# Optimization experiments

Measured on AMD Instinct MI355X. Metric: run time of the kernel, lower is better.

Reference implementation:

```python
import jax, jax.numpy as jnp
import numpy as np

N, E = 50000, 800000
C, NT, ET, H, D = 128, 8, 16, 64, 4
TOTAL_IN = 2 * C + 2 * NT + ET  # 288
EPS = 1e-5


def setup_inputs() -> dict:
    key = jax.random.key(0)
    ks = jax.random.split(key, 10)
    x = jax.random.normal(ks[0], (N, C), dtype=jnp.float32)
    edge_index = jax.random.randint(ks[1], (2, E), 0, N, dtype=jnp.int64)
    edge_types = jax.random.randint(ks[2], (E,), 0, ET, dtype=jnp.int64)
    node_types = jax.random.randint(ks[3], (N,), 0, NT, dtype=jnp.int64)
    ln_w = jnp.ones((TOTAL_IN,), dtype=jnp.float32)
    ln_b = jnp.zeros((TOTAL_IN,), dtype=jnp.float32)
    W1 = jax.random.normal(ks[4], (TOTAL_IN, H), dtype=jnp.float32) * 0.05
    b1 = jnp.zeros((H,), dtype=jnp.float32)
    W2 = jax.random.normal(ks[5], (H, D * D), dtype=jnp.float32) * 0.05
    b2 = jnp.zeros((D * D,), dtype=jnp.float32)
    return {"x": x, "edge_index": edge_index, "edge_types": edge_types,
            "node_types": node_types, "ln_w": ln_w, "ln_b": ln_b,
            "W1": W1, "b1": b1, "W2": W2, "b2": b2}


def reference(x, edge_index, edge_types, node_types, ln_w, ln_b, W1, b1, W2, b2):
    row, col = edge_index[0], edge_index[1]
    # edge gathers of node features and one-hot type encodings
    nt_oh = jax.nn.one_hot(node_types, NT, dtype=x.dtype)   # [N, NT]
    et_oh = jax.nn.one_hot(edge_types, ET, dtype=x.dtype)   # [E, ET]
    h = jnp.concatenate([x[row], x[col], nt_oh[row], nt_oh[col], et_oh], axis=-1)  # [E, 288]
    # LayerNorm
    mu = jnp.mean(h, axis=-1, keepdims=True)
    var = jnp.mean(jnp.square(h - mu), axis=-1, keepdims=True)
    h = (h - mu) * jax.lax.rsqrt(var + EPS) * ln_w + ln_b
    # small MLP
    h = jax.nn.relu(h @ W1 + b1) @ W2 + b2          # [E, D*D]
    h = h.reshape(-1, D, D)
    att = jax.nn.softmax(h, axis=-1)                 # row-stochastic per edge
    return jnp.eye(D, dtype=h.dtype)[None] - att     # [E, D, D]
```

## Files before the change

### kernel.cpp

```cpp
#include <hip/hip_runtime.h>
#include <hip/hip_bf16.h>

#define NN 50000
#define NE 800000
#define C 128
#define HH 64
#define TIN 288
#define LN_EPS 1e-5f

typedef __attribute__((ext_vector_type(8))) short bf16x8;
typedef __attribute__((ext_vector_type(4))) float f32x4;
typedef __attribute__((ext_vector_type(2))) float f32x2;
typedef __attribute__((ext_vector_type(4))) int i32x4;

#define ETT_OFF 512
#define B1F_OFF 2560
#define B2F_OFF 35328
#define OHU_OFF 37376
#define OHV_OFF 38400
#define SQ_OFF 39424
#define U_OFF 439424
#define V_OFF 3639424

__device__ __forceinline__ short f2bf(float f) {
    __hip_bfloat16 h = __float2bfloat16(f);
    return __builtin_bit_cast(short, h);
}
__device__ __forceinline__ float bf2f(short s) {
    unsigned int u = ((unsigned int)(unsigned short)s) << 16;
    return __builtin_bit_cast(float, u);
}

__global__ void prep_weights(const float* __restrict__ ln_w,
                             const float* __restrict__ ln_b,
                             const float* __restrict__ W1,
                             const float* __restrict__ b1,
                             const float* __restrict__ W2,
                             float* __restrict__ ws) {
    int gid = blockIdx.x * 256 + threadIdx.x;
    if (blockIdx.x == 0 && threadIdx.x < 64) {
        int l = threadIdx.x;
        float s = 0.f, c = 0.f;
        for (int k = 0; k < TIN; ++k) {
            float w = W1[k * HH + l];
            s += ln_w[k] * w;
            c += ln_b[k] * w;
        }
        ws[l] = s;
        ws[64 + l] = c + b1[l];
    }
    short* B1 = (short*)((char*)ws + B1F_OFF);
    for (int idx = gid; idx < 16384; idx += 8192) {
        int j = idx & 7, l = (idx >> 3) & 63, cc = (idx >> 9) & 3, kt = idx >> 11;
        int g = l >> 4, m = l & 15;
        int k = 32 * kt + 8 * g + j, n = 16 * cc + m;
        B1[idx] = f2bf(ln_w[k] * W1[k * HH + n]);
    }
    short* B2 = (short*)((char*)ws + B2F_OFF);
    for (int idx = gid; idx < 1024; idx += 8192) {
        int j = idx & 7, l = (idx >> 3) & 63, kt = idx >> 9;
        int g = l >> 4, m = l & 15;
        int k = 32 * kt + 8 * g + j;
        B2[idx] = f2bf(W2[k * 16 + m]);
    }
    short* ohu = (short*)((char*)ws + OHU_OFF);
    short* ohv = (short*)((char*)ws + OHV_OFF);
    for (int idx = gid; idx < 512; idx += 8192) {
        int t = idx >> 6, j = idx & 63;
        ohu[idx] = f2bf(ln_w[256 + t] * W1[(256 + t) * HH + j]);
        ohv[idx] = f2bf(ln_w[264 + t] * W1[(264 + t) * HH + j]);
    }
    short* ett = (short*)((char*)ws + ETT_OFF);
    for (int idx = gid; idx < 1024; idx += 8192) {
        int et = idx >> 6, j = idx & 63;
        int unit = (j >> 3) ^ (et & 7);
        ett[et * 64 + unit * 8 + (j & 7)] = f2bf(ln_w[272 + et] * W1[(272 + et) * HH + j]);
    }
}

__global__ __launch_bounds__(512) void node_uv(const float* __restrict__ x,
                                               const int* __restrict__ ntype,
                                               float* __restrict__ ws) {
    __shared__ __align__(16) char lds_n[32768 + 8192];
    int tid = threadIdx.x;
    {
        const f32x4* src = (const f32x4*)((const char*)ws + B1F_OFF);
        f32x4* dst = (f32x4*)lds_n;
        for (int i = tid; i < 2048; i += 512) dst[i] = src[i];
    }
    __syncthreads();

    int wave = tid >> 6, lane = tid & 63, m = lane & 15, g = lane >> 4;
    int tile = blockIdx.x * 128 + wave * 16;
    int n = tile + m;
    int nc = n < NN ? n : NN - 1;

    float sum = 0.f, sq = 0.f;
    bf16x8 a[4];
#pragma unroll
    for (int kt = 0; kt < 4; ++kt) {
        const float* p = x + (size_t)nc * C + kt * 32 + g * 8;
        f32x4 p0 = __builtin_nontemporal_load((const f32x4*)p);
        f32x4 p1 = __builtin_nontemporal_load((const f32x4*)(p + 4));
        float vv[8] = {p0[0], p0[1], p0[2], p0[3], p1[0], p1[1], p1[2], p1[3]};
#pragma unroll
        for (int j = 0; j < 8; ++j) {
            sum += vv[j];
            sq = fmaf(vv[j], vv[j], sq);
            a[kt][j] = f2bf(vv[j]);
        }
    }
    sum += __shfl_xor(sum, 16); sum += __shfl_xor(sum, 32);
    sq  += __shfl_xor(sq, 16);  sq  += __shfl_xor(sq, 32);
    if (g == 0 && n < NN)
        ((float2*)((char*)ws + SQ_OFF))[n] = make_float2(sum, sq);

    f32x4 au[4], av[4];
#pragma unroll
    for (int cc = 0; cc < 4; ++cc) { au[cc] = (f32x4){0,0,0,0}; av[cc] = (f32x4){0,0,0,0}; }
#pragma unroll
    for (int kt = 0; kt < 4; ++kt) {
        const bf16x8* Bu = (const bf16x8*)(lds_n + (kt * 4) * 1024);
        const bf16x8* Bv = (const bf16x8*)(lds_n + ((kt + 4) * 4) * 1024);
#pragma unroll
        for (int cc = 0; cc < 4; ++cc) {
            au[cc] = __builtin_amdgcn_mfma_f32_16x16x32_bf16(a[kt], Bu[cc * 64 + lane], au[cc], 0, 0, 0);
            av[cc] = __builtin_amdgcn_mfma_f32_16x16x32_bf16(a[kt], Bv[cc * 64 + lane], av[cc], 0, 0, 0);
        }
    }

    int ntv[4];
#pragma unroll
    for (int i = 0; i < 4; ++i) {
        int nn = tile + 4 * g + i;
        ntv[i] = ntype[nn < NN ? nn : NN - 1];
    }
    const unsigned short* ohu = (const unsigned short*)((const char*)ws + OHU_OFF);
    const unsigned short* ohv = (const unsigned short*)((const char*)ws + OHV_OFF);
    char* u8 = (char*)ws + U_OFF;
    char* v8 = (char*)ws + V_OFF;
    char* tb8 = lds_n + 32768 + wave * 1024;
    int nst = tile + m;
    int k2 = m >> 2;

#pragma unroll
    for (int cc = 0; cc < 4; ++cc)
#pragma unroll
        for (int i = 0; i < 4; ++i) {
            float val = au[cc][i] + bf2f((short)ohu[ntv[i] * 64 + 16 * cc + m]);
            int d = 16 * cc + m;
            int pos = (d < 32) ? (16 * (d >> 3) + (d & 7))
                               : (16 * ((d - 32) >> 3) + 8 + ((d - 32) & 7));
            pos ^= (g << 4);
            int pk = __builtin_amdgcn_cvt_pk_fp8_f32(val, val, 0, false);
            tb8[(4 * g + i) * 64 + pos] = (char)(pk & 0xFF);
        }
    if (nst < NN) {
        i32x4 val = *(const i32x4*)(tb8 + m * 64 + 16 * (g ^ k2));
        *(i32x4*)(u8 + (size_t)nst * 64 + 16 * g) = val;
    }
#pragma unroll
    for (int cc = 0; cc < 4; ++cc)
#pragma unroll
        for (int i = 0; i < 4; ++i) {
            float val = av[cc][i] + bf2f((short)ohv[ntv[i] * 64 + 16 * cc + m]);
            int d = 16 * cc + m;
            int pos = (d < 32) ? (16 * (d >> 3) + (d & 7))
                               : (16 * ((d - 32) >> 3) + 8 + ((d - 32) & 7));
            pos ^= (g << 4);
            int pk = __builtin_amdgcn_cvt_pk_fp8_f32(val, val, 0, false);
            tb8[(4 * g + i) * 64 + pos] = (char)(pk & 0xFF);
        }
    if (nst < NN) {
        i32x4 val = *(const i32x4*)(tb8 + m * 64 + 16 * (g ^ k2));
        *(i32x4*)(v8 + (size_t)nst * 64 + 16 * g) = val;
    }
}

__device__ __forceinline__ void dec4(int w, float* o) {
    f32x2 lo = __builtin_amdgcn_cvt_pk_f32_fp8(w, false);
    f32x2 hi = __builtin_amdgcn_cvt_pk_f32_fp8(w, true);
    o[0] = lo[0]; o[1] = lo[1]; o[2] = hi[0]; o[3] = hi[1];
}

__global__ __launch_bounds__(512) void edge_kernel(
    const int* __restrict__ ei,
    const int* __restrict__ etype,
    const float* __restrict__ ws,
    const float* __restrict__ b2,
    float* __restrict__ out) {
    __shared__ __align__(16) short lds_e[2048];
    int tid = threadIdx.x;
    int wave = tid >> 6, lane = tid & 63, m = lane & 15, g = lane >> 4;
    int base = blockIdx.x * 256 + wave * 32;
    int e0 = base + m, e1 = base + 16 + m;

    int row0 = __builtin_nontemporal_load(ei + e0);
    int col0 = __builtin_nontemporal_load(ei + NE + e0);
    int et0  = __builtin_nontemporal_load(etype + e0);
    int row1 = __builtin_nontemporal_load(ei + e1);
    int col1 = __builtin_nontemporal_load(ei + NE + e1);
    int et1  = __builtin_nontemporal_load(etype + e1);

    if (tid < 128)
        ((f32x4*)lds_e)[tid] = *(const f32x4*)((const char*)ws + B2F_OFF + tid * 16);
    else if (tid < 256)
        ((f32x4*)lds_e)[tid] = *(const f32x4*)((const char*)ws + ETT_OFF + (tid - 128) * 16);
    __syncthreads();

    const float2* SQ = (const float2*)((const char*)ws + SQ_OFF);
    float2 sqr0 = SQ[row0], sqc0 = SQ[col0];
    float2 sqr1 = SQ[row1], sqc1 = SQ[col1];
    const char* u8 = (const char*)ws + U_OFF;
    const char* v8 = (const char*)ws + V_OFF;
    i32x4 u0q = *(const i32x4*)(u8 + (size_t)row0 * 64 + 16 * g);
    i32x4 v0q = *(const i32x4*)(v8 + (size_t)col0 * 64 + 16 * g);
    i32x4 u1q = *(const i32x4*)(u8 + (size_t)row1 * 64 + 16 * g);
    i32x4 v1q = *(const i32x4*)(v8 + (size_t)col1 * 64 + 16 * g);
    f32x4 s00 = *(const f32x4*)(ws + 8 * g);
    f32x4 s01 = *(const f32x4*)(ws + 8 * g + 4);
    f32x4 s10 = *(const f32x4*)(ws + 32 + 8 * g);
    f32x4 s11 = *(const f32x4*)(ws + 36 + 8 * g);
    f32x4 c00 = *(const f32x4*)(ws + 64 + 8 * g);
    f32x4 c01 = *(const f32x4*)(ws + 64 + 8 * g + 4);
    f32x4 c10 = *(const f32x4*)(ws + 96 + 8 * g);
    f32x4 c11 = *(const f32x4*)(ws + 100 + 8 * g);
    f32x4 b2q = *(const f32x4*)(b2 + 4 * g);
    asm volatile("" ::: "memory");

    const bf16x8* W2A = (const bf16x8*)lds_e;
    bf16x8 w0 = W2A[lane], w1 = W2A[64 + lane];
    const short* ett = lds_e + 1024;

#pragma unroll
    for (int t = 0; t < 2; ++t) {
        int et = t ? et1 : et0;
        float2 sqr = t ? sqr1 : sqr0, sqc = t ? sqc1 : sqc0;
        i32x4 uq = t ? u1q : u0q;
        i32x4 vq = t ? v1q : v0q;

        bf16x8 T0 = *(const bf16x8*)(ett + et * 64 + ((g ^ (et & 7)) << 3));
        bf16x8 T1 = *(const bf16x8*)(ett + et * 64 + (((4 + g) ^ (et & 7)) << 3));

        float uf[16], vf[16];
        dec4(uq[0], uf); dec4(uq[1], uf + 4); dec4(uq[2], uf + 8); dec4(uq[3], uf + 12);
        dec4(vq[0], vf); dec4(vq[1], vf + 4); dec4(vq[2], vf + 8); dec4(vq[3], vf + 12);

        float mu = (sqr.x + sqc.x + 3.0f) * (1.0f / TIN);
        float var = (sqr.y + sqc.y + 3.0f) * (1.0f / TIN) - mu * mu;
        float rstd = rsqrtf(var + LN_EPS);
        float rm = rstd * mu;

        bf16x8 af0, af1;
#pragma unroll
        for (int j = 0; j < 4; ++j) {
            float tt = uf[j] + vf[j] + bf2f(T0[j]);
            float h = fmaf(rstd, tt, fmaf(-rm, s00[j], c00[j]));
            af0[j] = f2bf(fmaxf(h, 0.f));
            float tt2 = uf[j + 4] + vf[j + 4] + bf2f(T0[j + 4]);
            float h2 = fmaf(rstd, tt2, fmaf(-rm, s01[j], c01[j]));
            af0[j + 4] = f2bf(fmaxf(h2, 0.f));
            float tt3 = uf[j + 8] + vf[j + 8] + bf2f(T1[j]);
            float h3 = fmaf(rstd, tt3, fmaf(-rm, s10[j], c10[j]));
            af1[j] = f2bf(fmaxf(h3, 0.f));
            float tt4 = uf[j + 12] + vf[j + 12] + bf2f(T1[j + 4]);
            float h4 = fmaf(rstd, tt4, fmaf(-rm, s11[j], c11[j]));
            af1[j + 4] = f2bf(fmaxf(h4, 0.f));
        }

        f32x4 o = {0.f, 0.f, 0.f, 0.f};
        o = __builtin_amdgcn_mfma_f32_16x16x32_bf16(w0, af0, o, 0, 0, 0);
        o = __builtin_amdgcn_mfma_f32_16x16x32_bf16(w1, af1, o, 0, 0, 0);

        float v0 = o[0] + b2q[0], v1 = o[1] + b2q[1];
        float v2 = o[2] + b2q[2], v3 = o[3] + b2q[3];
        float mx = fmaxf(fmaxf(v0, v1), fmaxf(v2, v3));
        float x0 = __expf(v0 - mx), x1 = __expf(v1 - mx);
        float x2 = __expf(v2 - mx), x3 = __expf(v3 - mx);
        float inv = 1.0f / (x0 + x1 + x2 + x3);
        f32x4 res;
        res[0] = (g == 0 ? 1.0f : 0.0f) - x0 * inv;
        res[1] = (g == 1 ? 1.0f : 0.0f) - x1 * inv;
        res[2] = (g == 2 ? 1.0f : 0.0f) - x2 * inv;
        res[3] = (g == 3 ? 1.0f : 0.0f) - x3 * inv;
        __builtin_nontemporal_store(res, (f32x4*)(out + (size_t)(base + 16 * t + m) * 16 + 4 * g));
    }
}

extern "C" void kernel_launch(void* const* d_in, const int* in_sizes, int n_in,
                              void* d_out, int out_size, void* d_ws, size_t ws_size,
                              hipStream_t stream) {
    const float* x     = (const float*)d_in[0];
    const int*   ei    = (const int*)d_in[1];
    const int*   etype = (const int*)d_in[2];
    const int*   ntype = (const int*)d_in[3];
    const float* ln_w  = (const float*)d_in[4];
    const float* ln_b  = (const float*)d_in[5];
    const float* W1    = (const float*)d_in[6];
    const float* b1    = (const float*)d_in[7];
    const float* W2    = (const float*)d_in[8];
    const float* b2    = (const float*)d_in[9];
    float* out = (float*)d_out;
    float* ws  = (float*)d_ws;

    prep_weights<<<32, 256, 0, stream>>>(ln_w, ln_b, W1, b1, W2, ws);
    node_uv<<<(NN + 127) / 128, 512, 0, stream>>>(x, ntype, ws);
    edge_kernel<<<NE / 256, 512, 0, stream>>>(ei, etype, ws, b2, out);
}
```

Baseline: 69.43 us.

## Drop LDS staging in edge kernel, store node stats as half, parallelize prep reduction

The edge kernel no longer stages W2 and edge-type weights through shared memory with a block barrier. Each lane reads them straight from global memory and relies on the cache, and blocks shrink to 256 threads with an occupancy hint. Per-node sum and sum-of-squares are stored as half2 instead of float2, which halves the random-gather bytes per edge. This risks precision loss in the variance computation, since sum-of-squares near 128 in fp16 carries a rounding error of roughly 0.06. The prep kernel's 288-long dot products are also split across four thread groups and combined through shared memory.

New measurement: 72.06 us. +3.8%, slower.

```diff
diff --git a/kernel.cpp b/kernel.cpp
--- a/kernel.cpp
+++ b/kernel.cpp
@@ -1,5 +1,6 @@
 #include <hip/hip_runtime.h>
 #include <hip/hip_bf16.h>
+#include <hip/hip_fp16.h>
 
 #define NN 50000
 #define NE 800000
@@ -37,17 +38,25 @@
                              const float* __restrict__ b1,
                              const float* __restrict__ W2,
                              float* __restrict__ ws) {
-    int gid = blockIdx.x * 256 + threadIdx.x;
-    if (blockIdx.x == 0 && threadIdx.x < 64) {
-        int l = threadIdx.x;
+    __shared__ float rs[256], rc[256];
+    int tid = threadIdx.x;
+    int gid = blockIdx.x * 256 + tid;
+    if (blockIdx.x == 0) {
+        int col = tid & 63, part = tid >> 6;
         float s = 0.f, c = 0.f;
-        for (int k = 0; k < TIN; ++k) {
-            float w = W1[k * HH + l];
+        for (int k = part * 72; k < part * 72 + 72; ++k) {
+            float w = W1[k * HH + col];
             s += ln_w[k] * w;
             c += ln_b[k] * w;
         }
-        ws[l] = s;
-        ws[64 + l] = c + b1[l];
+        rs[tid] = s; rc[tid] = c;
+        __syncthreads();
+        if (tid < 64) {
+            float ss = rs[tid] + rs[64 + tid] + rs[128 + tid] + rs[192 + tid];
+            float cc = rc[tid] + rc[64 + tid] + rc[128 + tid] + rc[192 + tid];
+            ws[tid] = ss;
+            ws[64 + tid] = cc + b1[tid];
+        }
     }
     short* B1 = (short*)((char*)ws + B1F_OFF);
     for (int idx = gid; idx < 16384; idx += 8192) {
@@ -73,8 +82,7 @@
     short* ett = (short*)((char*)ws + ETT_OFF);
     for (int idx = gid; idx < 1024; idx += 8192) {
         int et = idx >> 6, j = idx & 63;
-        int unit = (j >> 3) ^ (et & 7);
-        ett[et * 64 + unit * 8 + (j & 7)] = f2bf(ln_w[272 + et] * W1[(272 + et) * HH + j]);
+        ett[idx] = f2bf(ln_w[272 + et] * W1[(272 + et) * HH + j]);
     }
 }
 
@@ -112,8 +120,12 @@
     }
     sum += __shfl_xor(sum, 16); sum += __shfl_xor(sum, 32);
     sq  += __shfl_xor(sq, 16);  sq  += __shfl_xor(sq, 32);
-    if (g == 0 && n < NN)
-        ((float2*)((char*)ws + SQ_OFF))[n] = make_float2(sum, sq);
+    if (g == 0 && n < NN) {
+        __half2 hp;
+        hp.x = __float2half(sum);
+        hp.y = __float2half(sq);
+        ((__half2*)((char*)ws + SQ_OFF))[n] = hp;
+    }
 
     f32x4 au[4], av[4];
 #pragma unroll
@@ -183,16 +195,15 @@
     o[0] = lo[0]; o[1] = lo[1]; o[2] = hi[0]; o[3] = hi[1];
 }
 
-__global__ __launch_bounds__(512) void edge_kernel(
+__global__ __launch_bounds__(256, 4) void edge_kernel(
     const int* __restrict__ ei,
     const int* __restrict__ etype,
     const float* __restrict__ ws,
     const float* __restrict__ b2,
     float* __restrict__ out) {
-    __shared__ __align__(16) short lds_e[2048];
     int tid = threadIdx.x;
     int wave = tid >> 6, lane = tid & 63, m = lane & 15, g = lane >> 4;
-    int base = blockIdx.x * 256 + wave * 32;
+    int base = blockIdx.x * 128 + wave * 32;
     int e0 = base + m, e1 = base + 16 + m;
 
     int row0 = __builtin_nontemporal_load(ei + e0);
@@ -202,21 +213,22 @@
     int col1 = __builtin_nontemporal_load(ei + NE + e1);
     int et1  = __builtin_nontemporal_load(etype + e1);
 
-    if (tid < 128)
-        ((f32x4*)lds_e)[tid] = *(const f32x4*)((const char*)ws + B2F_OFF + tid * 16);
-    else if (tid < 256)
-        ((f32x4*)lds_e)[tid] = *(const f32x4*)((const char*)ws + ETT_OFF + (tid - 128) * 16);
-    __syncthreads();
-
-    const float2* SQ = (const float2*)((const char*)ws + SQ_OFF);
-    float2 sqr0 = SQ[row0], sqc0 = SQ[col0];
-    float2 sqr1 = SQ[row1], sqc1 = SQ[col1];
+    const __half2* SQ = (const __half2*)((const char*)ws + SQ_OFF);
+    __half2 sr0 = SQ[row0], sc0h = SQ[col0];
+    __half2 sr1 = SQ[row1], sc1h = SQ[col1];
     const char* u8 = (const char*)ws + U_OFF;
     const char* v8 = (const char*)ws + V_OFF;
     i32x4 u0q = *(const i32x4*)(u8 + (size_t)row0 * 64 + 16 * g);
     i32x4 v0q = *(const i32x4*)(v8 + (size_t)col0 * 64 + 16 * g);
     i32x4 u1q = *(const i32x4*)(u8 + (size_t)row1 * 64 + 16 * g);
     i32x4 v1q = *(const i32x4*)(v8 + (size_t)col1 * 64 + 16 * g);
+    const unsigned short* ettg = (const unsigned short*)((const char*)ws + ETT_OFF);
+    bf16x8 T00 = *(const bf16x8*)(ettg + et0 * 64 + 8 * g);
+    bf16x8 T01 = *(const bf16x8*)(ettg + et0 * 64 + 32 + 8 * g);
+    bf16x8 T10 = *(const bf16x8*)(ettg + et1 * 64 + 8 * g);
+    bf16x8 T11 = *(const bf16x8*)(ettg + et1 * 64 + 32 + 8 * g);
+    const bf16x8* W2A = (const bf16x8*)((const char*)ws + B2F_OFF);
+    bf16x8 w0 = W2A[lane], w1 = W2A[64 + lane];
     f32x4 s00 = *(const f32x4*)(ws + 8 * g);
     f32x4 s01 = *(const f32x4*)(ws + 8 * g + 4);
     f32x4 s10 = *(const f32x4*)(ws + 32 + 8 * g);
@@ -228,26 +240,21 @@
     f32x4 b2q = *(const f32x4*)(b2 + 4 * g);
     asm volatile("" ::: "memory");
 
-    const bf16x8* W2A = (const bf16x8*)lds_e;
-    bf16x8 w0 = W2A[lane], w1 = W2A[64 + lane];
-    const short* ett = lds_e + 1024;
-
 #pragma unroll
     for (int t = 0; t < 2; ++t) {
-        int et = t ? et1 : et0;
-        float2 sqr = t ? sqr1 : sqr0, sqc = t ? sqc1 : sqc0;
+        __half2 sqr = t ? sr1 : sr0, sqc = t ? sc1h : sc0h;
         i32x4 uq = t ? u1q : u0q;
         i32x4 vq = t ? v1q : v0q;
-
-        bf16x8 T0 = *(const bf16x8*)(ett + et * 64 + ((g ^ (et & 7)) << 3));
-        bf16x8 T1 = *(const bf16x8*)(ett + et * 64 + (((4 + g) ^ (et & 7)) << 3));
+        bf16x8 T0 = t ? T10 : T00, T1 = t ? T11 : T01;
 
         float uf[16], vf[16];
         dec4(uq[0], uf); dec4(uq[1], uf + 4); dec4(uq[2], uf + 8); dec4(uq[3], uf + 12);
         dec4(vq[0], vf); dec4(vq[1], vf + 4); dec4(vq[2], vf + 8); dec4(vq[3], vf + 12);
 
-        float mu = (sqr.x + sqc.x + 3.0f) * (1.0f / TIN);
-        float var = (sqr.y + sqc.y + 3.0f) * (1.0f / TIN) - mu * mu;
+        float sums = __half2float(sqr.x) + __half2float(sqc.x) + 3.0f;
+        float sqs  = __half2float(sqr.y) + __half2float(sqc.y) + 3.0f;
+        float mu = sums * (1.0f / TIN);
+        float var = sqs * (1.0f / TIN) - mu * mu;
         float rstd = rsqrtf(var + LN_EPS);
         float rm = rstd * mu;
 
@@ -305,5 +312,5 @@
 
     prep_weights<<<32, 256, 0, stream>>>(ln_w, ln_b, W1, b1, W2, ws);
     node_uv<<<(NN + 127) / 128, 512, 0, stream>>>(x, ntype, ws);
-    edge_kernel<<<NE / 256, 512, 0, stream>>>(ei, etype, ws, b2, out);
-}
+    edge_kernel<<<NE / 128, 256, 0, stream>>>(ei, etype, ws, b2, out);
+}
```
